# Kernel optimization log

Hardware: AMD Instinct MI355X
Metric: run time of the kernel (lower is better)

Reference implementation:

```python
import jax, jax.numpy as jnp
import numpy as np

HEADS = 8
DIM_HEAD = 64
DIM = 512
TOP_K = -1  # -1 -> L_context // heads
EPS_LN = 1e-5
EPS_L2 = 1e-12


def chan_ln(x, g):
    # channel LayerNorm over axis 1 of [B, C, H, W], unbiased=False variance
    mean = x.mean(axis=1, keepdims=True)
    var = x.var(axis=1, keepdims=True)
    return (x - mean) * jax.lax.rsqrt(var + EPS_LN) * g[None, :, None, None]


def l2norm(x, axis):
    n = jnp.linalg.norm(x, axis=axis, keepdims=True)
    return x / jnp.maximum(n, EPS_L2)


def conv1x1(x, w):
    # w: [out_c, in_c], x: [B, in_c, H, W]
    return jnp.einsum('oc,bchw->bohw', w, x)


def select_kv(q, k, v, top_k, key):
    # q: [BH, Lq, d]; k, v: [BH, Lkv, d]
    BH, Lq, d = q.shape
    idx_rand = jax.random.randint(key, (BH, top_k), 0, Lq)
    q_small = jnp.take_along_axis(q, idx_rand[:, :, None], axis=1)  # [BH, top_k, d]

    def per(args):
        k_b, qs_b = args  # [Lkv, d], [top_k, d]
        dist = jnp.sum(jnp.abs(k_b[:, None, :] - qs_b[None, :, :]), axis=-1)  # L1 cdist [Lkv, top_k]
        min_dist = dist.min(axis=1)  # [Lkv]
        _, idx = jax.lax.top_k(-min_dist, top_k)  # smallest distances
        return idx

    idx = jax.lax.map(per, (k, q_small))  # [BH, top_k]
    sel_k = jnp.take_along_axis(k, idx[:, :, None], axis=1)
    sel_v = jnp.take_along_axis(v, idx[:, :, None], axis=1)
    return sel_k, sel_v


def setup_inputs() -> dict:
    key = jax.random.key(0)
    ks = jax.random.split(key, 8)
    B, H, W = 8, 48, 48
    inner = HEADS * DIM_HEAD
    return {
        'query_source': jax.random.normal(ks[0], (B, DIM, H, W), jnp.float32),
        'context': jax.random.normal(ks[1], (B, DIM, H, W), jnp.float32),
        'g_ctx': jnp.ones((DIM,), jnp.float32),
        'g_qs': jnp.ones((DIM,), jnp.float32),
        'g_outn': jnp.ones((DIM,), jnp.float32),
        'w_kv': jax.random.normal(ks[2], (2 * inner, DIM), jnp.float32) * (DIM ** -0.5),
        'w_q': jax.random.normal(ks[3], (inner, DIM), jnp.float32) * (DIM ** -0.5),
        'w_out': jax.random.normal(ks[4], (DIM, inner), jnp.float32) * (inner ** -0.5),
        'gamma': jnp.full((1,), 0.5, jnp.float32),
    }


def reference(query_source, context, g_ctx, g_qs, g_outn, w_kv, w_q, w_out, gamma):
    b, c, hq, wq = query_source.shape
    hc, wc = context.shape[2], context.shape[3]
    inner = HEADS * DIM_HEAD

    ctx = chan_ln(context, g_ctx)
    qs = chan_ln(query_source, g_qs)

    kv = conv1x1(ctx, w_kv)            # [b, 2*inner, hc, wc]
    k, v = kv[:, :inner], kv[:, inner:]
    q = conv1x1(qs, w_q)               # [b, inner, hq, wq]

    # fold heads: [b, heads, dim_head, H, W]
    q = q.reshape(b, HEADS, DIM_HEAD, hq, wq)
    k = k.reshape(b, HEADS, DIM_HEAD, hc, wc)
    v = v.reshape(b, HEADS, DIM_HEAD, hc, wc)

    # l2 normalize over the per-head channel dim (original: F.normalize(dim=1) on [(bh), d, H, W])
    q = l2norm(q, axis=2)
    k = l2norm(k, axis=2)

    # flatten spatial: [b, heads, L, d]
    q = q.reshape(b, HEADS, DIM_HEAD, hq * wq).transpose(0, 1, 3, 2)
    k = k.reshape(b, HEADS, DIM_HEAD, hc * wc).transpose(0, 1, 3, 2)
    v = v.reshape(b, HEADS, DIM_HEAD, hc * wc).transpose(0, 1, 3, 2)

    L_ctx = k.shape[2]
    top_k = TOP_K if TOP_K > 0 else L_ctx // HEADS
    if top_k < L_ctx:
        BH = b * HEADS
        sk, sv = select_kv(q.reshape(BH, -1, DIM_HEAD),
                           k.reshape(BH, -1, DIM_HEAD),
                           v.reshape(BH, -1, DIM_HEAD),
                           top_k, jax.random.key(42))
        k = sk.reshape(b, HEADS, top_k, DIM_HEAD)
        v = sv.reshape(b, HEADS, top_k, DIM_HEAD)

    # SDPA with scale=1.0, no mask, eval (dropout 0)
    scores = jnp.einsum('bhqd,bhkd->bhqk', q, k)
    attn = jax.nn.softmax(scores, axis=-1)
    out = jnp.einsum('bhqk,bhkd->bhqd', attn, v)

    # [b, heads, L, d] -> [b, heads*dim_head, hq, wq]
    out = out.transpose(0, 1, 3, 2).reshape(b, inner, hq, wq)
    out = conv1x1(out, w_out)
    out = chan_ln(out, g_outn)
    return gamma * out + query_source
```

## Files before the change

### kernel.cpp

```cpp
#include <hip/hip_runtime.h>
#include <hip/hip_bf16.h>

#define BB 8
#define CC 512
#define LLOC 2304
#define NHEADS 8
#define DH 64
#define BH 64
#define TKSEL 288

typedef unsigned int u32;
typedef short short8 __attribute__((ext_vector_type(8)));
typedef float f32x4 __attribute__((ext_vector_type(4)));

__device__ inline unsigned short f2bf(float f) {
  unsigned u = __float_as_uint(f);
  u += 0x7FFFu + ((u >> 16) & 1u);
  return (unsigned short)(u >> 16);
}
__device__ inline float b2f(unsigned short h) {
  return __uint_as_float(((unsigned)h) << 16);
}

#define GLOAD_LDS(gsrc, ldst) \
  __builtin_amdgcn_global_load_lds((const __attribute__((address_space(1))) u32*)(gsrc), \
                                   (__attribute__((address_space(3))) u32*)(ldst), 16, 0, 0)

__global__ __launch_bounds__(256) void k_ln_stats(const float* __restrict__ x,
                                                  float* __restrict__ st) {
  int b = blockIdx.y;
  int lx = threadIdx.x & 63;
  int cg = threadIdx.x >> 6;
  int loc = blockIdx.x * 64 + lx;
  const float* xb = x + (size_t)b * CC * LLOC;
  float s = 0.f, s2 = 0.f;
  for (int c = cg; c < CC; c += 4) {
    float v = xb[(size_t)c * LLOC + loc];
    s += v; s2 += v * v;
  }
  __shared__ float sh[2][256];
  sh[0][threadIdx.x] = s; sh[1][threadIdx.x] = s2;
  __syncthreads();
  if (threadIdx.x < 64) {
    int t = threadIdx.x;
    float S  = sh[0][t] + sh[0][t+64] + sh[0][t+128] + sh[0][t+192];
    float S2 = sh[1][t] + sh[1][t+64] + sh[1][t+128] + sh[1][t+192];
    float mean = S * (1.f/512.f);
    float var  = S2 * (1.f/512.f) - mean * mean;
    float rstd = 1.f / sqrtf(var + 1e-5f);
    size_t o = ((size_t)b * LLOC + blockIdx.x*64 + t) * 2;
    st[o] = mean; st[o+1] = rstd;
  }
}

__device__ inline void tf2x32(unsigned ks0, unsigned ks1, unsigned x0, unsigned x1,
                              unsigned& y0, unsigned& y1) {
  unsigned ks2 = ks0 ^ ks1 ^ 0x1BD11BDAu;
#define TF_R(r) { x0 += x1; x1 = (x1 << (r)) | (x1 >> (32-(r))); x1 ^= x0; }
  x0 += ks0; x1 += ks1;
  TF_R(13) TF_R(15) TF_R(26) TF_R(6)
  x0 += ks1; x1 += ks2 + 1u;
  TF_R(17) TF_R(29) TF_R(16) TF_R(24)
  x0 += ks2; x1 += ks0 + 2u;
  TF_R(13) TF_R(15) TF_R(26) TF_R(6)
  x0 += ks0; x1 += ks1 + 3u;
  TF_R(17) TF_R(29) TF_R(16) TF_R(24)
  x0 += ks1; x1 += ks2 + 4u;
  TF_R(13) TF_R(15) TF_R(26) TF_R(6)
  x0 += ks2; x1 += ks0 + 5u;
#undef TF_R
  y0 = x0; y1 = x1;
}

__global__ __launch_bounds__(256) void k_threefry(int* __restrict__ idxRand) {
  unsigned i = blockIdx.x * 256 + threadIdx.x;
  if (i >= 18432u) return;
  unsigned a0, a1, b0, b1;
  tf2x32(0u, 42u, 0u, 0u, a0, a1);
  tf2x32(0u, 42u, 0u, 1u, b0, b1);
  unsigned h0, h1, l0, l1;
  tf2x32(a0, a1, 0u, i, h0, h1);
  tf2x32(b0, b1, 0u, i, l0, l1);
  unsigned h = h0 ^ h1;
  unsigned l = l0 ^ l1;
  const unsigned span = 2304u;
  idxRand[i] = (int)(((h % span) * 256u + (l % span)) % span);
}

__global__ __launch_bounds__(256) void k_prep_w(const float* __restrict__ W,
    const float* __restrict__ G, unsigned short* __restrict__ Wh,
    unsigned short* __restrict__ Wl, int total) {
  int i = (blockIdx.x * 256 + threadIdx.x) * 2;
  if (i >= total) return;
  int c = i & 511;
  float2 w2 = *(const float2*)&W[i];
  float g0 = G ? G[c] : 1.f, g1 = G ? G[c+1] : 1.f;
  float f0 = w2.x * g0, f1 = w2.y * g1;
  unsigned short h0 = f2bf(f0), h1 = f2bf(f1);
  unsigned short q0 = f2bf(f0 - b2f(h0)), q1 = f2bf(f1 - b2f(h1));
  *(unsigned*)&Wh[i] = (unsigned)h0 | ((unsigned)h1 << 16);
  *(unsigned*)&Wl[i] = (unsigned)q0 | ((unsigned)q1 << 16);
}

__global__ __launch_bounds__(256) void k_prep_x(const float* __restrict__ X,
    const float* __restrict__ stats, unsigned short* __restrict__ Xh,
    unsigned short* __restrict__ Xl) {
  int b = blockIdx.z, c0 = blockIdx.y * 64, loc0 = blockIdx.x * 64;
  int t = threadIdx.x;
  __shared__ float sm[64][65];
  int lx = t & 63;
  float mean = stats[((size_t)b * LLOC + loc0 + lx) * 2];
  float rstd = stats[((size_t)b * LLOC + loc0 + lx) * 2 + 1];
#pragma unroll
  for (int i = 0; i < 16; ++i) {
    int c = (t >> 6) + i * 4;
    float v = X[((size_t)b * CC + c0 + c) * LLOC + loc0 + lx];
    sm[c][lx] = (v - mean) * rstd;
  }
  __syncthreads();
  int loc = t >> 2, cs = (t & 3) * 16;
  unsigned uh[8], ul[8];
#pragma unroll
  for (int j = 0; j < 8; ++j) {
    float f0 = sm[cs + j*2][loc];
    float f1 = sm[cs + j*2 + 1][loc];
    unsigned short h0 = f2bf(f0), h1 = f2bf(f1);
    unsigned short q0 = f2bf(f0 - b2f(h0)), q1 = f2bf(f1 - b2f(h1));
    uh[j] = (unsigned)h0 | ((unsigned)h1 << 16);
    ul[j] = (unsigned)q0 | ((unsigned)q1 << 16);
  }
  size_t base = ((size_t)b * LLOC + loc0 + loc) * 512 + c0 + cs;
  *(uint4*)(Xh + base)     = make_uint4(uh[0], uh[1], uh[2], uh[3]);
  *(uint4*)(Xh + base + 8) = make_uint4(uh[4], uh[5], uh[6], uh[7]);
  *(uint4*)(Xl + base)     = make_uint4(ul[0], ul[1], ul[2], ul[3]);
  *(uint4*)(Xl + base + 8) = make_uint4(ul[4], ul[5], ul[6], ul[7]);
}

__global__ __launch_bounds__(256) void k_mfma3(
    const unsigned short* __restrict__ Wh, const unsigned short* __restrict__ Wl,
    const unsigned short* __restrict__ Xh, const unsigned short* __restrict__ Xl,
    float* __restrict__ dst) {
  int b = blockIdx.z;
  int o0 = blockIdx.y * 128, loc0 = blockIdx.x * 128;
  int t = threadIdx.x, l = t & 63, w = t >> 6;
  int wr = w >> 1, wc = w & 1;
  __shared__ unsigned short Ah[128*64], Al[128*64], Bh[128*64], Bl[128*64];
  f32x4 acc[4][4];
#pragma unroll
  for (int i = 0; i < 4; ++i)
#pragma unroll
    for (int j = 0; j < 4; ++j) acc[i][j] = (f32x4){0.f, 0.f, 0.f, 0.f};

  const char* WhC = (const char*)Wh;
  const char* WlC = (const char*)Wl;
  const char* XhC = (const char*)(Xh + (size_t)b * LLOC * 512);
  const char* XlC = (const char*)(Xl + (size_t)b * LLOC * 512);
  int srow = l >> 3;
  int schunk = (l & 7) ^ srow;

  for (int kt = 0; kt < 8; ++kt) {
    int kb = kt * 128;
#pragma unroll
    for (int j = 0; j < 4; ++j) {
      int r = w * 32 + j * 8;
      size_t arow = (size_t)(o0 + r + srow) * 1024 + kb + schunk * 16;
      size_t brow = (size_t)(loc0 + r + srow) * 1024 + kb + schunk * 16;
      GLOAD_LDS(WhC + arow, ((char*)Ah) + r * 128);
      GLOAD_LDS(WlC + arow, ((char*)Al) + r * 128);
      GLOAD_LDS(XhC + brow, ((char*)Bh) + r * 128);
      GLOAD_LDS(XlC + brow, ((char*)Bl) + r * 128);
    }
    __syncthreads();
#pragma unroll
    for (int ks = 0; ks < 2; ++ks) {
      short8 ah[4], al[4], bh[4], bl[4];
#pragma unroll
      for (int ot = 0; ot < 4; ++ot) {
        int row = wr * 64 + ot * 16 + (l & 15);
        int off = row * 128 + ((ks * 4 + (l >> 4)) ^ (row & 7)) * 16;
        ah[ot] = *(const short8*)(((const char*)Ah) + off);
        al[ot] = *(const short8*)(((const char*)Al) + off);
      }
#pragma unroll
      for (int bt = 0; bt < 4; ++bt) {
        int row = wc * 64 + bt * 16 + (l & 15);
        int off = row * 128 + ((ks * 4 + (l >> 4)) ^ (row & 7)) * 16;
        bh[bt] = *(const short8*)(((const char*)Bh) + off);
        bl[bt] = *(const short8*)(((const char*)Bl) + off);
      }
#pragma unroll
      for (int ot = 0; ot < 4; ++ot)
#pragma unroll
        for (int bt = 0; bt < 4; ++bt) {
          acc[ot][bt] = __builtin_amdgcn_mfma_f32_16x16x32_bf16(ah[ot], bh[bt], acc[ot][bt], 0, 0, 0);
          acc[ot][bt] = __builtin_amdgcn_mfma_f32_16x16x32_bf16(ah[ot], bl[bt], acc[ot][bt], 0, 0, 0);
          acc[ot][bt] = __builtin_amdgcn_mfma_f32_16x16x32_bf16(al[ot], bh[bt], acc[ot][bt], 0, 0, 0);
        }
    }
    __syncthreads();
  }
#pragma unroll
  for (int ot = 0; ot < 4; ++ot) {
    int ob = o0 + wr * 64 + ot * 16 + (l >> 4) * 4;
#pragma unroll
    for (int bt = 0; bt < 4; ++bt) {
      int loc = loc0 + wc * 64 + bt * 16 + (l & 15);
#pragma unroll
      for (int r = 0; r < 4; ++r) {
        int od = ob + r;
        dst[(((size_t)(b * NHEADS + (od >> 6))) * LLOC + loc) * DH + (od & 63)] = acc[ot][bt][r];
      }
    }
  }
}

__global__ __launch_bounds__(256) void k_mfma1(int mode,
    const unsigned short* __restrict__ W, const unsigned short* __restrict__ X,
    float* __restrict__ outF, unsigned short* __restrict__ outU) {
  int b = blockIdx.z;
  int o0 = blockIdx.y * 128, loc0 = blockIdx.x * 128;
  int t = threadIdx.x, l = t & 63, w = t >> 6;
  int wr = w >> 1, wc = w & 1;
  __shared__ unsigned short Asm[128*64], Bsm[128*64];
  f32x4 acc[4][4];
#pragma unroll
  for (int i = 0; i < 4; ++i)
#pragma unroll
    for (int j = 0; j < 4; ++j) acc[i][j] = (f32x4){0.f, 0.f, 0.f, 0.f};
  const char* Wc = (const char*)W;
  const char* Xc = (const char*)(X + (size_t)b * LLOC * 512);
  int srow = l >> 3;
  int schunk = (l & 7) ^ srow;
  for (int kt = 0; kt < 8; ++kt) {
    int kb = kt * 128;
#pragma unroll
    for (int j = 0; j < 4; ++j) {
      int r = w * 32 + j * 8;
      GLOAD_LDS(Wc + (size_t)(o0 + r + srow) * 1024 + kb + schunk * 16,
                ((char*)Asm) + r * 128);
      GLOAD_LDS(Xc + (size_t)(loc0 + r + srow) * 1024 + kb + schunk * 16,
                ((char*)Bsm) + r * 128);
    }
    __syncthreads();
#pragma unroll
    for (int ks = 0; ks < 2; ++ks) {
      short8 af[4], bf[4];
#pragma unroll
      for (int ot = 0; ot < 4; ++ot) {
        int row = wr * 64 + ot * 16 + (l & 15);
        af[ot] = *(const short8*)(((const char*)Asm) + row * 128 + (((ks*4 + (l>>4)) ^ (row&7)) * 16));
      }
#pragma unroll
      for (int bt = 0; bt < 4; ++bt) {
        int row = wc * 64 + bt * 16 + (l & 15);
        bf[bt] = *(const short8*)(((const char*)Bsm) + row * 128 + (((ks*4 + (l>>4)) ^ (row&7)) * 16));
      }
#pragma unroll
      for (int ot = 0; ot < 4; ++ot)
#pragma unroll
        for (int bt = 0; bt < 4; ++bt)
          acc[ot][bt] = __builtin_amdgcn_mfma_f32_16x16x32_bf16(af[ot], bf[bt], acc[ot][bt], 0, 0, 0);
    }
    __syncthreads();
  }
#pragma unroll
  for (int ot = 0; ot < 4; ++ot) {
    int ob = o0 + wr * 64 + ot * 16 + (l >> 4) * 4;
#pragma unroll
    for (int bt = 0; bt < 4; ++bt) {
      int loc = loc0 + wc * 64 + bt * 16 + (l & 15);
#pragma unroll
      for (int r = 0; r < 4; ++r) {
        int o = ob + r;
        float v = acc[ot][bt][r];
        if (mode == 2)
          outF[((size_t)b * CC + o) * LLOC + loc] = v;
        else
          outU[(((size_t)(b * NHEADS + (o >> 6))) * LLOC + loc) * DH + (o & 63)] = f2bf(v);
      }
    }
  }
}

__global__ __launch_bounds__(256) void k_l2norm(float* __restrict__ Q, float* __restrict__ K,
                                                unsigned short* __restrict__ Qb) {
  size_t gid = (size_t)blockIdx.x * 256 + threadIdx.x;
  size_t vec = gid >> 6;
  int lane = threadIdx.x & 63;
  float* buf = (blockIdx.y == 0) ? Q : K;
  float v = buf[vec * 64 + lane];
  float ss = v * v;
#pragma unroll
  for (int o = 32; o >= 1; o >>= 1) ss += __shfl_xor(ss, o, 64);
  float n = sqrtf(ss);
  float vn = v / fmaxf(n, 1e-12f);
  buf[vec * 64 + lane] = vn;
  if (blockIdx.y == 0)
    Qb[vec * 64 + ((((lane >> 3) ^ ((int)vec & 7)) << 3) | (lane & 7))] = f2bf(vn);
}

__global__ __launch_bounds__(256) void k_mindist(const float* __restrict__ K,
    const float* __restrict__ Q, const int* __restrict__ idxRand,
    float* __restrict__ mindP) {
  int chunk = blockIdx.x, row = blockIdx.y, jz = blockIdx.z;
  __shared__ float qs[72][64];
  int kk = chunk * 256 + threadIdx.x;
  float kv[64];
  const float* kp = &K[((size_t)row * LLOC + kk) * 64];
#pragma unroll
  for (int d = 0; d < 64; d++) kv[d] = kp[d];
  for (int e = threadIdx.x; e < 72 * 16; e += 256) {
    int j = e >> 4, t4 = (e & 15) * 4;
    int qi = idxRand[row * TKSEL + jz * 72 + j];
    *(float4*)&qs[j][t4] = *(const float4*)&Q[((size_t)row * LLOC + qi) * 64 + t4];
  }
  __syncthreads();
  float best = 3.402823e38f;
  for (int j = 0; j < 72; j++) {
    float s = 0.f;
#pragma unroll
    for (int d = 0; d < 64; d++) s += fabsf(kv[d] - qs[j][d]);
    best = fminf(best, s);
  }
  mindP[((size_t)jz * BH + row) * LLOC + kk] = best;
}

__global__ __launch_bounds__(256) void k_select(const float* __restrict__ mindP,
                                                int* __restrict__ sel) {
  int row = blockIdx.y;
  int i = blockIdx.x * 256 + threadIdx.x;
  __shared__ float dd[LLOC];
  const size_t stride = (size_t)BH * LLOC;
  for (int e = threadIdx.x; e < LLOC; e += 256) {
    size_t o = (size_t)row * LLOC + e;
    float m0 = fminf(mindP[o], mindP[o + stride]);
    float m1 = fminf(mindP[o + 2 * stride], mindP[o + 3 * stride]);
    dd[e] = fminf(m0, m1);
  }
  __syncthreads();
  float di = dd[i];
  int rank = 0;
  for (int j = 0; j < LLOC; j += 4) {
    float4 dj = *(const float4*)&dd[j];
    rank += (dj.x < di) || (dj.x == di && (j+0) < i);
    rank += (dj.y < di) || (dj.y == di && (j+1) < i);
    rank += (dj.z < di) || (dj.z == di && (j+2) < i);
    rank += (dj.w < di) || (dj.w == di && (j+3) < i);
  }
  if (rank < TKSEL) sel[row * TKSEL + rank] = i;
}

__global__ __launch_bounds__(256) void k_gather(const float* __restrict__ K,
    const unsigned short* __restrict__ Vb, const int* __restrict__ sel,
    unsigned short* __restrict__ Kc, unsigned short* __restrict__ Vt) {
  int row = blockIdx.x;
  int d = threadIdx.x & 63;
  for (int ki = threadIdx.x >> 6; ki < TKSEL; ki += 4) {
    int k = sel[row * TKSEL + ki];
    float kv = K[((size_t)row * LLOC + k) * 64 + d];
    Kc[((size_t)row * TKSEL + ki) * 64 + (((d >> 3) ^ (ki & 7)) << 3) + (d & 7)] = f2bf(kv);
    Vt[((size_t)row * 64 + d) * TKSEL + ki] = Vb[((size_t)row * LLOC + k) * 64 + d];
  }
}

__global__ __launch_bounds__(256) void k_attn_mfma(
    const unsigned short* __restrict__ Qb, const unsigned short* __restrict__ Kc,
    const unsigned short* __restrict__ Vt, unsigned short* __restrict__ AOb) {
  int row = blockIdx.y, q0 = blockIdx.x * 64;
  int t = threadIdx.x, l = t & 63, w = t >> 6;
  int q15 = l & 15, l4 = l >> 4;
  __shared__ unsigned short Qsm[64 * 64];
  __shared__ unsigned short Ksm[96 * 64];
  __shared__ unsigned short Vsm[64 * 120];
  __shared__ unsigned short Psm[4 * 512];

  f32x4 oacc[4];
#pragma unroll
  for (int dt = 0; dt < 4; ++dt) oacc[dt] = (f32x4){0.f, 0.f, 0.f, 0.f};
  float lsum = 0.f;

  const char* QbC = (const char*)(Qb + ((size_t)row * LLOC + q0) * 64);
#pragma unroll
  for (int i = 0; i < 2; ++i)
    GLOAD_LDS(QbC + (size_t)(i * 256 + w * 64 + l) * 16, ((char*)Qsm) + (i * 256 + w * 64) * 16);

  for (int c = 0; c < 3; ++c) {
    const char* KcC = (const char*)(Kc + (((size_t)row * TKSEL) + c * 96) * 64);
#pragma unroll
    for (int i = 0; i < 3; ++i)
      GLOAD_LDS(KcC + (size_t)(i * 256 + w * 64 + l) * 16, ((char*)Ksm) + (i * 256 + w * 64) * 16);
#pragma unroll
    for (int i = 0; i < 3; ++i) {
      int s = i * 256 + t;
      int d = s / 12, j = s % 12;
      uint4 v = *(const uint4*)(Vt + ((size_t)row * 64 + d) * TKSEL + c * 96 + j * 8);
      *(uint4*)((char*)Vsm + d * 240 + j * 16) = v;
    }
    __syncthreads();

    f32x4 sacc[6];
#pragma unroll
    for (int kt = 0; kt < 6; ++kt) sacc[kt] = (f32x4){0.f, 0.f, 0.f, 0.f};
#pragma unroll
    for (int ks = 0; ks < 2; ++ks) {
      int qrow = w * 16 + q15;
      short8 qf = *(const short8*)(Qsm + qrow * 64 + (((ks * 4 + l4) ^ (qrow & 7)) << 3));
#pragma unroll
      for (int kt = 0; kt < 6; ++kt) {
        int krow = kt * 16 + q15;
        short8 kf = *(const short8*)(Ksm + krow * 64 + (((ks * 4 + l4) ^ (krow & 7)) << 3));
        sacc[kt] = __builtin_amdgcn_mfma_f32_16x16x32_bf16(kf, qf, sacc[kt], 0, 0, 0);
      }
    }

    char* Pw = (char*)(Psm + w * 512);
#pragma unroll
    for (int s3 = 0; s3 < 3; ++s3) {
#pragma unroll
      for (int h2 = 0; h2 < 2; ++h2) {
        int kt = 2 * s3 + h2;
        float p0 = expf(sacc[kt][0]), p1 = expf(sacc[kt][1]);
        float p2 = expf(sacc[kt][2]), p3 = expf(sacc[kt][3]);
        lsum += (p0 + p1) + (p2 + p3);
        unsigned lo = (unsigned)f2bf(p0) | ((unsigned)f2bf(p1) << 16);
        unsigned hi = (unsigned)f2bf(p2) | ((unsigned)f2bf(p3) << 16);
        int sl = (h2 * 4 + l4) ^ ((q15 & 3) << 1);
        *(uint2*)(Pw + q15 * 64 + sl * 8) = make_uint2(lo, hi);
      }
      short8 pB = *(const short8*)(Pw + q15 * 64 + (((2 * l4) ^ ((q15 & 3) << 1)) * 8));
#pragma unroll
      for (int dt = 0; dt < 4; ++dt) {
        short8 vA = *(const short8*)(Vsm + (dt * 16 + q15) * 120 + s3 * 32 + l4 * 8);
        oacc[dt] = __builtin_amdgcn_mfma_f32_16x16x32_bf16(vA, pB, oacc[dt], 0, 0, 0);
      }
    }
    __syncthreads();
  }

  lsum += __shfl_xor(lsum, 16, 64);
  lsum += __shfl_xor(lsum, 32, 64);
  float inv = 1.f / lsum;
  int bq = row >> 3, hq = row & 7;
  int loc = q0 + w * 16 + q15;
  unsigned short* op = AOb + ((size_t)bq * LLOC + loc) * 512 + hq * 64;
#pragma unroll
  for (int dt = 0; dt < 4; ++dt) {
    unsigned w0 = (unsigned)f2bf(oacc[dt][0] * inv) | ((unsigned)f2bf(oacc[dt][1] * inv) << 16);
    unsigned w1 = (unsigned)f2bf(oacc[dt][2] * inv) | ((unsigned)f2bf(oacc[dt][3] * inv) << 16);
    *(uint2*)(op + dt * 16 + l4 * 4) = make_uint2(w0, w1);
  }
}

__global__ __launch_bounds__(256) void k_final(const float* __restrict__ CO,
    const float* __restrict__ st, const float* __restrict__ g,
    const float* __restrict__ gamma, const float* __restrict__ qsrc,
    float* __restrict__ out) {
  size_t i = (size_t)blockIdx.x * 256 + threadIdx.x;
  int loc = (int)(i % LLOC);
  int c = (int)((i / LLOC) % CC);
  int b = (int)(i / ((size_t)LLOC * CC));
  float mean = st[((size_t)b * LLOC + loc) * 2];
  float rstd = st[((size_t)b * LLOC + loc) * 2 + 1];
  float v = (CO[i] - mean) * rstd * g[c];
  out[i] = gamma[0] * v + qsrc[i];
}

extern "C" void kernel_launch(void* const* d_in, const int* in_sizes, int n_in,
                              void* d_out, int out_size, void* d_ws, size_t ws_size,
                              hipStream_t stream) {
  const float* qsrc  = (const float*)d_in[0];
  const float* ctx   = (const float*)d_in[1];
  const float* g_ctx = (const float*)d_in[2];
  const float* g_qs  = (const float*)d_in[3];
  const float* g_out = (const float*)d_in[4];
  const float* w_kv  = (const float*)d_in[5];
  const float* w_q   = (const float*)d_in[6];
  const float* w_out = (const float*)d_in[7];
  const float* gamma = (const float*)d_in[8];
  float* out = (float*)d_out;

  float* ws = (float*)d_ws;
  float* statsCtx = ws;
  float* statsQs  = ws + 36864;
  int*   idxRand  = (int*)(ws + 73728);
  int*   sel      = (int*)(ws + 92160);
  float* Q  = ws + 258048;
  float* K  = Q + 9437184;
  unsigned short* usb = (unsigned short*)(K + 9437184);
  unsigned short* Vb     = usb;
  unsigned short* Xt_hi  = Vb + 9437184;
  unsigned short* Xt_lo  = Xt_hi + 9437184;
  unsigned short* Wkv_hi = Xt_lo + 9437184;
  unsigned short* Wkv_lo = Wkv_hi + 524288;
  unsigned short* Wq_hi  = Wkv_lo + 524288;
  unsigned short* Wq_lo  = Wq_hi + 262144;
  unsigned short* Wo_hi  = Wq_lo + 262144;
  unsigned short* Wo_lo  = Wo_hi + 262144;
  float* mindP = (float*)(Wo_lo + 262144);
  unsigned short* Kc = (unsigned short*)(mindP + 589824);
  unsigned short* Vt = Kc + 1179648;
  unsigned short* Qb = Xt_lo;
  float* CO = Q;

  k_ln_stats<<<dim3(36, 8), 256, 0, stream>>>(ctx, statsCtx);
  k_ln_stats<<<dim3(36, 8), 256, 0, stream>>>(qsrc, statsQs);
  k_threefry<<<72, 256, 0, stream>>>(idxRand);
  k_prep_w<<<1024, 256, 0, stream>>>(w_kv, g_ctx, Wkv_hi, Wkv_lo, 1024 * 512);
  k_prep_w<<<512, 256, 0, stream>>>(w_q, g_qs, Wq_hi, Wq_lo, 512 * 512);
  k_prep_w<<<512, 256, 0, stream>>>(w_out, nullptr, Wo_hi, Wo_lo, 512 * 512);
  k_prep_x<<<dim3(36, 8, 8), 256, 0, stream>>>(ctx, statsCtx, Xt_hi, Xt_lo);
  k_mfma3<<<dim3(18, 4, 8), 256, 0, stream>>>(Wkv_hi, Wkv_lo, Xt_hi, Xt_lo, K);
  k_mfma1<<<dim3(18, 4, 8), 256, 0, stream>>>(3, Wkv_hi + 512*512, Xt_hi, nullptr, Vb);
  k_prep_x<<<dim3(36, 8, 8), 256, 0, stream>>>(qsrc, statsQs, Xt_hi, Xt_lo);
  k_mfma3<<<dim3(18, 4, 8), 256, 0, stream>>>(Wq_hi, Wq_lo, Xt_hi, Xt_lo, Q);
  k_l2norm<<<dim3(36864, 2), 256, 0, stream>>>(Q, K, Qb);
  k_mindist<<<dim3(9, 64, 4), 256, 0, stream>>>(K, Q, idxRand, mindP);
  k_select<<<dim3(9, 64), 256, 0, stream>>>(mindP, sel);
  k_gather<<<64, 256, 0, stream>>>(K, Vb, sel, Kc, Vt);
  k_attn_mfma<<<dim3(36, 64), 256, 0, stream>>>(Qb, Kc, Vt, Xt_hi);
  k_mfma1<<<dim3(18, 4, 8), 256, 0, stream>>>(2, Wo_hi, Xt_hi, CO, nullptr);
  k_ln_stats<<<dim3(36, 8), 256, 0, stream>>>(CO, statsCtx);
  k_final<<<36864, 256, 0, stream>>>(CO, statsCtx, g_out, gamma, qsrc, out);
}
```

Baseline: 766.8 us.

## Fuse L2 normalization into Q/K projection epilogue and retile mindist kernel

The per-head L2 normalization, plus the swizzled bf16 Q copy, moves into the epilogue of the split-bf16 MFMA projection kernel. Each wave owns one 64-wide head, so the squared norm is reduced across lanes with two shuffles. This removes a separate full read and write pass over Q and K. The min-distance kernel is also reworked so each thread handles two keys and two queries per step using float4 loads and 192-thread blocks, which raises register reuse at some cost in occupancy. Qb moves to its own workspace region instead of aliasing Xt_lo.

```diff
diff --git a/kernel.cpp b/kernel.cpp
--- a/kernel.cpp
+++ b/kernel.cpp
@@ -139,7 +139,7 @@
 __global__ __launch_bounds__(256) void k_mfma3(
     const unsigned short* __restrict__ Wh, const unsigned short* __restrict__ Wl,
     const unsigned short* __restrict__ Xh, const unsigned short* __restrict__ Xl,
-    float* __restrict__ dst) {
+    float* __restrict__ dst, unsigned short* __restrict__ Qb) {
   int b = blockIdx.z;
   int o0 = blockIdx.y * 128, loc0 = blockIdx.x * 128;
   int t = threadIdx.x, l = t & 63, w = t >> 6;
@@ -199,18 +199,28 @@
     }
     __syncthreads();
   }
-#pragma unroll
-  for (int ot = 0; ot < 4; ++ot) {
-    int ob = o0 + wr * 64 + ot * 16 + (l >> 4) * 4;
-#pragma unroll
-    for (int bt = 0; bt < 4; ++bt) {
-      int loc = loc0 + wc * 64 + bt * 16 + (l & 15);
+  int head = (o0 >> 6) + wr;
+#pragma unroll
+  for (int bt = 0; bt < 4; ++bt) {
+    float ss = 0.f;
+#pragma unroll
+    for (int ot = 0; ot < 4; ++ot)
+#pragma unroll
+      for (int r = 0; r < 4; ++r) ss += acc[ot][bt][r] * acc[ot][bt][r];
+    ss += __shfl_xor(ss, 16, 64);
+    ss += __shfl_xor(ss, 32, 64);
+    float sc = 1.f / fmaxf(sqrtf(ss), 1e-12f);
+    int loc = loc0 + wc * 64 + bt * 16 + (l & 15);
+    size_t vecbase = (((size_t)(b * NHEADS + head)) * LLOC + loc) * DH;
+#pragma unroll
+    for (int ot = 0; ot < 4; ++ot)
 #pragma unroll
       for (int r = 0; r < 4; ++r) {
-        int od = ob + r;
-        dst[(((size_t)(b * NHEADS + (od >> 6))) * LLOC + loc) * DH + (od & 63)] = acc[ot][bt][r];
-      }
-    }
+        int d = ot * 16 + (l >> 4) * 4 + r;
+        float v = acc[ot][bt][r] * sc;
+        dst[vecbase + d] = v;
+        if (Qb) Qb[vecbase + ((((d >> 3) ^ (loc & 7)) << 3) | (d & 7))] = f2bf(v);
+      }
   }
 }
 
@@ -282,47 +292,46 @@
   }
 }
 
-__global__ __launch_bounds__(256) void k_l2norm(float* __restrict__ Q, float* __restrict__ K,
-                                                unsigned short* __restrict__ Qb) {
-  size_t gid = (size_t)blockIdx.x * 256 + threadIdx.x;
-  size_t vec = gid >> 6;
-  int lane = threadIdx.x & 63;
-  float* buf = (blockIdx.y == 0) ? Q : K;
-  float v = buf[vec * 64 + lane];
-  float ss = v * v;
-#pragma unroll
-  for (int o = 32; o >= 1; o >>= 1) ss += __shfl_xor(ss, o, 64);
-  float n = sqrtf(ss);
-  float vn = v / fmaxf(n, 1e-12f);
-  buf[vec * 64 + lane] = vn;
-  if (blockIdx.y == 0)
-    Qb[vec * 64 + ((((lane >> 3) ^ ((int)vec & 7)) << 3) | (lane & 7))] = f2bf(vn);
-}
-
-__global__ __launch_bounds__(256) void k_mindist(const float* __restrict__ K,
+__global__ __launch_bounds__(192, 3) void k_mindist(const float* __restrict__ K,
     const float* __restrict__ Q, const int* __restrict__ idxRand,
     float* __restrict__ mindP) {
-  int chunk = blockIdx.x, row = blockIdx.y, jz = blockIdx.z;
+  int c6 = blockIdx.x, row = blockIdx.y, jz = blockIdx.z;
   __shared__ float qs[72][64];
-  int kk = chunk * 256 + threadIdx.x;
-  float kv[64];
-  const float* kp = &K[((size_t)row * LLOC + kk) * 64];
-#pragma unroll
-  for (int d = 0; d < 64; d++) kv[d] = kp[d];
-  for (int e = threadIdx.x; e < 72 * 16; e += 256) {
+  int t = threadIdx.x;
+  int k0 = c6 * 384 + t;
+  float4 kv0[16], kv1[16];
+  const float4* kp0 = (const float4*)&K[((size_t)row * LLOC + k0) * 64];
+  const float4* kp1 = (const float4*)&K[((size_t)row * LLOC + k0 + 192) * 64];
+#pragma unroll
+  for (int d = 0; d < 16; ++d) { kv0[d] = kp0[d]; kv1[d] = kp1[d]; }
+  for (int e = t; e < 72 * 16; e += 192) {
     int j = e >> 4, t4 = (e & 15) * 4;
     int qi = idxRand[row * TKSEL + jz * 72 + j];
     *(float4*)&qs[j][t4] = *(const float4*)&Q[((size_t)row * LLOC + qi) * 64 + t4];
   }
   __syncthreads();
-  float best = 3.402823e38f;
-  for (int j = 0; j < 72; j++) {
-    float s = 0.f;
-#pragma unroll
-    for (int d = 0; d < 64; d++) s += fabsf(kv[d] - qs[j][d]);
-    best = fminf(best, s);
-  }
-  mindP[((size_t)jz * BH + row) * LLOC + kk] = best;
+  float bA = 3.402823e38f, bB = 3.402823e38f;
+  for (int j = 0; j < 72; j += 2) {
+    float sA0 = 0.f, sA1 = 0.f, sB0 = 0.f, sB1 = 0.f;
+#pragma unroll
+    for (int d = 0; d < 16; ++d) {
+      float4 q0 = *(const float4*)&qs[j][d * 4];
+      float4 q1 = *(const float4*)&qs[j + 1][d * 4];
+      sA0 += (fabsf(kv0[d].x - q0.x) + fabsf(kv0[d].y - q0.y)) +
+             (fabsf(kv0[d].z - q0.z) + fabsf(kv0[d].w - q0.w));
+      sA1 += (fabsf(kv0[d].x - q1.x) + fabsf(kv0[d].y - q1.y)) +
+             (fabsf(kv0[d].z - q1.z) + fabsf(kv0[d].w - q1.w));
+      sB0 += (fabsf(kv1[d].x - q0.x) + fabsf(kv1[d].y - q0.y)) +
+             (fabsf(kv1[d].z - q0.z) + fabsf(kv1[d].w - q0.w));
+      sB1 += (fabsf(kv1[d].x - q1.x) + fabsf(kv1[d].y - q1.y)) +
+             (fabsf(kv1[d].z - q1.z) + fabsf(kv1[d].w - q1.w));
+    }
+    bA = fminf(bA, fminf(sA0, sA1));
+    bB = fminf(bB, fminf(sB0, sB1));
+  }
+  size_t base = ((size_t)jz * BH + row) * LLOC + k0;
+  mindP[base]       = bA;
+  mindP[base + 192] = bB;
 }
 
 __global__ __launch_bounds__(256) void k_select(const float* __restrict__ mindP,
@@ -499,7 +508,7 @@
   float* mindP = (float*)(Wo_lo + 262144);
   unsigned short* Kc = (unsigned short*)(mindP + 589824);
   unsigned short* Vt = Kc + 1179648;
-  unsigned short* Qb = Xt_lo;
+  unsigned short* Qb = Vt + 1179648;
   float* CO = Q;
 
   k_ln_stats<<<dim3(36, 8), 256, 0, stream>>>(ctx, statsCtx);
@@ -509,12 +518,11 @@
   k_prep_w<<<512, 256, 0, stream>>>(w_q, g_qs, Wq_hi, Wq_lo, 512 * 512);
   k_prep_w<<<512, 256, 0, stream>>>(w_out, nullptr, Wo_hi, Wo_lo, 512 * 512);
   k_prep_x<<<dim3(36, 8, 8), 256, 0, stream>>>(ctx, statsCtx, Xt_hi, Xt_lo);
-  k_mfma3<<<dim3(18, 4, 8), 256, 0, stream>>>(Wkv_hi, Wkv_lo, Xt_hi, Xt_lo, K);
+  k_mfma3<<<dim3(18, 4, 8), 256, 0, stream>>>(Wkv_hi, Wkv_lo, Xt_hi, Xt_lo, K, nullptr);
   k_mfma1<<<dim3(18, 4, 8), 256, 0, stream>>>(3, Wkv_hi + 512*512, Xt_hi, nullptr, Vb);
   k_prep_x<<<dim3(36, 8, 8), 256, 0, stream>>>(qsrc, statsQs, Xt_hi, Xt_lo);
-  k_mfma3<<<dim3(18, 4, 8), 256, 0, stream>>>(Wq_hi, Wq_lo, Xt_hi, Xt_lo, Q);
-  k_l2norm<<<dim3(36864, 2), 256, 0, stream>>>(Q, K, Qb);
-  k_mindist<<<dim3(9, 64, 4), 256, 0, stream>>>(K, Q, idxRand, mindP);
+  k_mfma3<<<dim3(18, 4, 8), 256, 0, stream>>>(Wq_hi, Wq_lo, Xt_hi, Xt_lo, Q, Qb);
+  k_mindist<<<dim3(6, 64, 4), 192, 0, stream>>>(K, Q, idxRand, mindP);
   k_select<<<dim3(9, 64), 256, 0, stream>>>(mindP, sel);
   k_gather<<<64, 256, 0, stream>>>(K, Vb, sel, Kc, Vt);
   k_attn_mfma<<<dim3(36, 64), 256, 0, stream>>>(Qb, Kc, Vt, Xt_hi);
```

Measured after the change: 725.1 us. -5.4%, faster.
